# Optimization experiments

Hardware: AMD Instinct MI355X
Metric: run time of the kernel (lower is better)

Reference implementation:

```python
import jax, jax.numpy as jnp
import numpy as np

N = 50000   # nodes
E = 800000  # edges
D = 64      # attrs_dim
H = 128     # 2*attrs_dim (GIN MLP hidden)
L = 3       # gnn_layers_num
G = 128     # graphs in batch


def setup_inputs() -> dict:
    key = jax.random.key(0)
    ks = jax.random.split(key, 9)
    s = 0.1
    attrs = jax.random.normal(ks[0], (N, D), dtype=jnp.float32)
    edge_index = jax.random.randint(ks[1], (2, E), 0, N, dtype=jnp.int64)
    batch = jnp.sort(jax.random.randint(ks[2], (N,), 0, G, dtype=jnp.int64))
    W1 = jax.random.normal(ks[3], (L, D, H), dtype=jnp.float32) * s
    b1 = jnp.zeros((L, H), jnp.float32)
    W2 = jax.random.normal(ks[4], (L, H, H), dtype=jnp.float32) * s
    b2 = jnp.zeros((L, H), jnp.float32)
    W3 = jax.random.normal(ks[5], (L, H, D), dtype=jnp.float32) * s
    b3 = jnp.zeros((L, D), jnp.float32)
    return {"attrs": attrs, "W1": W1, "b1": b1, "W2": W2, "b2": b2,
            "W3": W3, "b3": b3, "edge_index": edge_index, "batch": batch}


def reference(attrs, W1, b1, W2, b2, W3, b3, edge_index, batch):
    src, dst = edge_index[0], edge_index[1]
    x = attrs
    for l in range(L):  # small fixed layer count
        # GINConv with eps=0: MLP(x + sum_{j->i} x_j)
        agg = jax.ops.segment_sum(x[src], dst, num_segments=N)
        h = x + agg
        # MLP with tanh after each linear (per MLP.forward)
        h = jnp.tanh(h @ W1[l] + b1[l])
        h = jnp.tanh(h @ W2[l] + b2[l])
        h = jnp.tanh(h @ W3[l] + b3[l])
        # outer activation in GNN.forward
        x = jnp.tanh(h)
    # scatter_mean over graph ids
    sums = jax.ops.segment_sum(x, batch, num_segments=G)          # [G, D]
    counts = jax.ops.segment_sum(jnp.ones((N,), x.dtype), batch, num_segments=G)
    return sums / jnp.maximum(counts, 1.0)[:, None]
```

## Files before the change

### kernel.cpp

```cpp
#include <hip/hip_runtime.h>
#include <math.h>

#define N_NODES 50000
#define N_EDGES 800000
#define DIM 64
#define HID 128
#define LAYERS 3
#define NGRAPH 128

#define SCAN_TILE 1024
#define SCAN_NB ((N_NODES + SCAN_TILE - 1) / SCAN_TILE)

#define POOL_ROWS 256
#define POOL_NB ((N_NODES + POOL_ROWS - 1) / POOL_ROWS)

typedef __attribute__((ext_vector_type(8))) short short8v;
typedef __attribute__((ext_vector_type(4))) float f32x4;

__device__ __forceinline__ float bf2f(unsigned short u) {
    return __uint_as_float(((unsigned)u) << 16);
}
__device__ __forceinline__ unsigned short f2bf(float x) {
    unsigned u = __float_as_uint(x);
    unsigned r = (u + 0x7fff + ((u >> 16) & 1)) >> 16;
    return (unsigned short)r;
}
__device__ __forceinline__ float fast_tanh(float x) {
    float xc = fminf(fmaxf(x, -9.0f), 9.0f);
    float y = __expf(2.0f * xc);
    return 1.0f - 2.0f * __builtin_amdgcn_rcpf(y + 1.0f);
}

__global__ void count_kernel(const int* __restrict__ dst,
                             int* __restrict__ counts,
                             unsigned short* __restrict__ rank) {
    int e = blockIdx.x * blockDim.x + threadIdx.x;
    if (e >= N_EDGES) return;
    rank[e] = (unsigned short)atomicAdd(&counts[dst[e]], 1);
}

__global__ void scan_partial_kernel(const int* __restrict__ counts,
                                    int* __restrict__ bsum) {
    __shared__ int red[256];
    const int b = blockIdx.x, tid = threadIdx.x;
    const int base = b * SCAN_TILE + tid * 4;
    int s = 0;
    if (base + 3 < N_NODES) {
        int4 v = *reinterpret_cast<const int4*>(counts + base);
        s = v.x + v.y + v.z + v.w;
    } else {
        for (int i = 0; i < 4; ++i)
            if (base + i < N_NODES) s += counts[base + i];
    }
    red[tid] = s;
    __syncthreads();
    for (int off = 128; off > 0; off >>= 1) {
        if (tid < off) red[tid] += red[tid + off];
        __syncthreads();
    }
    if (tid == 0) bsum[b] = red[0];
}

__global__ void scan_mid_kernel(const int* __restrict__ bsum,
                                int* __restrict__ bpre,
                                int* __restrict__ offsets) {
    int tid = threadIdx.x;
    int orig = (tid < SCAN_NB) ? bsum[tid] : 0;
    int v = orig;
    for (int off = 1; off < 64; off <<= 1) {
        int u = __shfl_up(v, off);
        if (tid >= off) v += u;
    }
    if (tid < SCAN_NB) bpre[tid] = v - orig;
    if (tid == 0) offsets[N_NODES] = N_EDGES;
}

__global__ void scan_final_kernel(const int* __restrict__ counts,
                                  const int* __restrict__ bpre,
                                  int* __restrict__ offsets) {
    __shared__ int pre[256];
    const int b = blockIdx.x, tid = threadIdx.x;
    const int base = b * SCAN_TILE + tid * 4;
    int c[4];
    int s = 0;
#pragma unroll
    for (int i = 0; i < 4; ++i) {
        c[i] = (base + i < N_NODES) ? counts[base + i] : 0;
        s += c[i];
    }
    pre[tid] = s;
    __syncthreads();
    for (int off = 1; off < 256; off <<= 1) {
        int v = (tid >= off) ? pre[tid - off] : 0;
        __syncthreads();
        pre[tid] += v;
        __syncthreads();
    }
    int run = bpre[b] + pre[tid] - s;
#pragma unroll
    for (int i = 0; i < 4; ++i) {
        if (base + i < N_NODES) {
            offsets[base + i] = run;
            run += c[i];
        }
    }
}

__global__ void place_kernel(const int* __restrict__ src,
                             const int* __restrict__ dst,
                             const unsigned short* __restrict__ rank,
                             const int* __restrict__ offsets,
                             unsigned short* __restrict__ csr_src) {
    int e = blockIdx.x * blockDim.x + threadIdx.x;
    if (e >= N_EDGES) return;
    csr_src[offsets[dst[e]] + (int)rank[e]] = (unsigned short)src[e];
}

template<int K, int C>
__global__ void repack_kernel(const float* __restrict__ W, unsigned short* __restrict__ P) {
    constexpr int KT = K / 32, CT = C / 16;
    int t = blockIdx.x * 256 + threadIdx.x;
    if (t >= LAYERS * KT * CT * 64) return;
    int lane = t & 63; int rest = t >> 6;
    int ct = rest % CT; rest /= CT;
    int kt = rest % KT; int l = rest / KT;
    int li = lane & 15, hi = lane >> 4;
    const float* Wl = W + (size_t)l * K * C;
    short8v o;
#pragma unroll
    for (int j = 0; j < 8; ++j)
        o[j] = (short)f2bf(Wl[(size_t)(kt * 32 + hi * 8 + j) * C + ct * 16 + li]);
    *reinterpret_cast<short8v*>(P + ((size_t)l * KT * CT * 64 + (size_t)(kt * CT + ct) * 64 + lane) * 8) = o;
}

template<bool F32IN>
__global__ __launch_bounds__(256) void gnn_layer_kernel(
        const float* __restrict__ xf, const unsigned short* __restrict__ xb,
        const int* __restrict__ offsets, const unsigned short* __restrict__ csr_src,
        const unsigned short* __restrict__ pw1, const float* __restrict__ bias1,
        const unsigned short* __restrict__ pw2, const float* __restrict__ bias2,
        const unsigned short* __restrict__ pw3, const float* __restrict__ bias3,
        unsigned short* __restrict__ outx) {
    __shared__ float aggA[16 * 68];
    __shared__ float aggB[16 * 68];
    __shared__ unsigned short tileA[16 * 128];
    __shared__ unsigned short tileB[16 * 128];
    __shared__ int soff[17];
    const int tid = threadIdx.x;
    const int wave = tid >> 6, lane = tid & 63;
    const int li = lane & 15, hi = lane >> 4;
    const int r0 = blockIdx.x * 16;
    char* tA = reinterpret_cast<char*>(tileA);
    char* tB = reinterpret_cast<char*>(tileB);

    if (tid < 17) soff[tid] = offsets[r0 + tid];
    __syncthreads();

    {
        const int g  = tid >> 3;
        const int nr = g >> 1;
        const int h  = g & 1;
        const int q  = tid & 7;
        const int n  = r0 + nr;
        float a[8];
        if (h == 0) {
            if (F32IN) {
                const float* xr = xf + (size_t)n * DIM + q * 8;
                float4 u = *reinterpret_cast<const float4*>(xr);
                float4 w = *reinterpret_cast<const float4*>(xr + 4);
                a[0]=u.x; a[1]=u.y; a[2]=u.z; a[3]=u.w;
                a[4]=w.x; a[5]=w.y; a[6]=w.z; a[7]=w.w;
            } else {
                short8v v = *reinterpret_cast<const short8v*>(xb + (size_t)n * DIM + q * 8);
#pragma unroll
                for (int j = 0; j < 8; ++j) a[j] = bf2f((unsigned short)v[j]);
            }
        } else {
#pragma unroll
            for (int j = 0; j < 8; ++j) a[j] = 0.f;
        }
        const int p0 = soff[nr], pe1 = soff[nr + 1];
        const int mid = p0 + ((pe1 - p0 + 1) >> 1);
        int p        = h ? mid : p0;
        const int pe = h ? pe1 : mid;
        for (; p + 4 <= pe; p += 4) {
            int s0 = csr_src[p + 0];
            int s1 = csr_src[p + 1];
            int s2 = csr_src[p + 2];
            int s3 = csr_src[p + 3];
            if (F32IN) {
                const float* x0 = xf + (size_t)s0 * DIM + q * 8;
                const float* x1 = xf + (size_t)s1 * DIM + q * 8;
                const float* x2 = xf + (size_t)s2 * DIM + q * 8;
                const float* x3 = xf + (size_t)s3 * DIM + q * 8;
                float4 u0 = *reinterpret_cast<const float4*>(x0);
                float4 w0 = *reinterpret_cast<const float4*>(x0 + 4);
                float4 u1 = *reinterpret_cast<const float4*>(x1);
                float4 w1 = *reinterpret_cast<const float4*>(x1 + 4);
                float4 u2 = *reinterpret_cast<const float4*>(x2);
                float4 w2 = *reinterpret_cast<const float4*>(x2 + 4);
                float4 u3 = *reinterpret_cast<const float4*>(x3);
                float4 w3 = *reinterpret_cast<const float4*>(x3 + 4);
                a[0] += u0.x + u1.x + u2.x + u3.x;
                a[1] += u0.y + u1.y + u2.y + u3.y;
                a[2] += u0.z + u1.z + u2.z + u3.z;
                a[3] += u0.w + u1.w + u2.w + u3.w;
                a[4] += w0.x + w1.x + w2.x + w3.x;
                a[5] += w0.y + w1.y + w2.y + w3.y;
                a[6] += w0.z + w1.z + w2.z + w3.z;
                a[7] += w0.w + w1.w + w2.w + w3.w;
            } else {
                short8v v0 = *reinterpret_cast<const short8v*>(xb + (size_t)s0 * DIM + q * 8);
                short8v v1 = *reinterpret_cast<const short8v*>(xb + (size_t)s1 * DIM + q * 8);
                short8v v2 = *reinterpret_cast<const short8v*>(xb + (size_t)s2 * DIM + q * 8);
                short8v v3 = *reinterpret_cast<const short8v*>(xb + (size_t)s3 * DIM + q * 8);
#pragma unroll
                for (int j = 0; j < 8; ++j)
                    a[j] += bf2f((unsigned short)v0[j]) + bf2f((unsigned short)v1[j])
                          + bf2f((unsigned short)v2[j]) + bf2f((unsigned short)v3[j]);
            }
        }
        for (; p < pe; ++p) {
            int s = csr_src[p];
            if (F32IN) {
                const float* xs = xf + (size_t)s * DIM + q * 8;
                float4 u = *reinterpret_cast<const float4*>(xs);
                float4 w = *reinterpret_cast<const float4*>(xs + 4);
                a[0] += u.x; a[1] += u.y; a[2] += u.z; a[3] += u.w;
                a[4] += w.x; a[5] += w.y; a[6] += w.z; a[7] += w.w;
            } else {
                short8v v = *reinterpret_cast<const short8v*>(xb + (size_t)s * DIM + q * 8);
#pragma unroll
                for (int j = 0; j < 8; ++j) a[j] += bf2f((unsigned short)v[j]);
            }
        }
        float* d = (h ? aggB : aggA) + nr * 68 + q * 8;
        *reinterpret_cast<f32x4*>(d)     = (f32x4){a[0], a[1], a[2], a[3]};
        *reinterpret_cast<f32x4*>(d + 4) = (f32x4){a[4], a[5], a[6], a[7]};
    }
    __syncthreads();

    short8v af[2];
#pragma unroll
    for (int kt = 0; kt < 2; ++kt) {
        const float* sA = &aggA[li * 68 + kt * 32 + hi * 8];
        const float* sB = &aggB[li * 68 + kt * 32 + hi * 8];
#pragma unroll
        for (int j = 0; j < 8; ++j) af[kt][j] = (short)f2bf(sA[j] + sB[j]);
    }

    f32x4 acc1[2];
#pragma unroll
    for (int c = 0; c < 2; ++c) acc1[c] = (f32x4){0.f, 0.f, 0.f, 0.f};
#pragma unroll
    for (int c = 0; c < 2; ++c) {
        const int ct = 2 * wave + c;
#pragma unroll
        for (int kt = 0; kt < 2; ++kt) {
            short8v bfr = *reinterpret_cast<const short8v*>(pw1 + ((size_t)(kt * 8 + ct) * 64 + lane) * 8);
            acc1[c] = __builtin_amdgcn_mfma_f32_16x16x32_bf16(af[kt], bfr, acc1[c], 0, 0, 0);
        }
    }
#pragma unroll
    for (int c = 0; c < 2; ++c) {
        const int ct = 2 * wave + c;
        float bv = bias1[ct * 16 + li];
#pragma unroll
        for (int j = 0; j < 4; ++j) {
            int row = hi * 4 + j;
            unsigned off = (unsigned)(row * 256 + (ct * 16 + li) * 2) ^ ((unsigned)(row & 7) << 4);
            *reinterpret_cast<unsigned short*>(tA + off) = f2bf(fast_tanh(acc1[c][j] + bv));
        }
    }
    __syncthreads();

    short8v af2[4];
#pragma unroll
    for (int kt = 0; kt < 4; ++kt) {
        unsigned off = (unsigned)(li * 256 + (kt * 32 + hi * 8) * 2) ^ ((unsigned)(li & 7) << 4);
        af2[kt] = *reinterpret_cast<const short8v*>(tA + off);
    }
    f32x4 acc2[2];
#pragma unroll
    for (int c = 0; c < 2; ++c) acc2[c] = (f32x4){0.f, 0.f, 0.f, 0.f};
#pragma unroll
    for (int c = 0; c < 2; ++c) {
        const int ct = 2 * wave + c;
#pragma unroll
        for (int kt = 0; kt < 4; ++kt) {
            short8v bfr = *reinterpret_cast<const short8v*>(pw2 + ((size_t)(kt * 8 + ct) * 64 + lane) * 8);
            acc2[c] = __builtin_amdgcn_mfma_f32_16x16x32_bf16(af2[kt], bfr, acc2[c], 0, 0, 0);
        }
    }
#pragma unroll
    for (int c = 0; c < 2; ++c) {
        const int ct = 2 * wave + c;
        float bv = bias2[ct * 16 + li];
#pragma unroll
        for (int j = 0; j < 4; ++j) {
            int row = hi * 4 + j;
            unsigned off = (unsigned)(row * 256 + (ct * 16 + li) * 2) ^ ((unsigned)(row & 7) << 4);
            *reinterpret_cast<unsigned short*>(tB + off) = f2bf(fast_tanh(acc2[c][j] + bv));
        }
    }
    __syncthreads();

    short8v af3[4];
#pragma unroll
    for (int kt = 0; kt < 4; ++kt) {
        unsigned off = (unsigned)(li * 256 + (kt * 32 + hi * 8) * 2) ^ ((unsigned)(li & 7) << 4);
        af3[kt] = *reinterpret_cast<const short8v*>(tB + off);
    }
    f32x4 acc3 = (f32x4){0.f, 0.f, 0.f, 0.f};
#pragma unroll
    for (int kt = 0; kt < 4; ++kt) {
        short8v bfr = *reinterpret_cast<const short8v*>(pw3 + ((size_t)(kt * 4 + wave) * 64 + lane) * 8);
        acc3 = __builtin_amdgcn_mfma_f32_16x16x32_bf16(af3[kt], bfr, acc3, 0, 0, 0);
    }
    {
        float bv = bias3[wave * 16 + li];
#pragma unroll
        for (int j = 0; j < 4; ++j) {
            int row = r0 + hi * 4 + j;
            float v = fast_tanh(fast_tanh(acc3[j] + bv));
            outx[(size_t)row * DIM + wave * 16 + li] = f2bf(v);
        }
    }
}

__global__ void pool_partial_kernel(const unsigned short* __restrict__ x,
                                    const int* __restrict__ batch,
                                    float* __restrict__ sums) {
    const int tid = threadIdx.x;
    const int d = tid & 63;
    const int rg = tid >> 6;
    int row = blockIdx.x * POOL_ROWS + rg;
    const int rowend = min(N_NODES, (blockIdx.x + 1) * POOL_ROWS);
    float acc = 0.f;
    int cur = -1;
    for (; row < rowend; row += 4) {
        int g = batch[row];
        if (g != cur) {
            if (cur >= 0) atomicAdd(&sums[cur * DIM + d], acc);
            acc = 0.f;
            cur = g;
        }
        acc += bf2f(x[(size_t)row * DIM + d]);
    }
    if (cur >= 0) atomicAdd(&sums[cur * DIM + d], acc);
}

__global__ void pool_final_kernel(const float* __restrict__ sums,
                                  const int* __restrict__ batch,
                                  float* __restrict__ out) {
    const int g = blockIdx.x;
    const int d = threadIdx.x;
    int lo = 0, hi = N_NODES;
    while (lo < hi) { int m = (lo + hi) >> 1; if (batch[m] < g) lo = m + 1; else hi = m; }
    int start = lo;
    hi = N_NODES;
    while (lo < hi) { int m = (lo + hi) >> 1; if (batch[m] < g + 1) lo = m + 1; else hi = m; }
    float cnt = (float)(lo - start);
    out[g * DIM + d] = sums[g * DIM + d] / fmaxf(cnt, 1.f);
}

extern "C" void kernel_launch(void* const* d_in, const int* in_sizes, int n_in,
                              void* d_out, int out_size, void* d_ws, size_t ws_size,
                              hipStream_t stream) {
    const float* attrs = (const float*)d_in[0];
    const float* W1    = (const float*)d_in[1];
    const float* b1    = (const float*)d_in[2];
    const float* W2    = (const float*)d_in[3];
    const float* b2    = (const float*)d_in[4];
    const float* W3    = (const float*)d_in[5];
    const float* b3    = (const float*)d_in[6];
    const int* edge_index = (const int*)d_in[7];
    const int* batch      = (const int*)d_in[8];
    float* out = (float*)d_out;

    unsigned short* buf0 = (unsigned short*)d_ws;
    unsigned short* buf1 = buf0 + (size_t)N_NODES * DIM;
    unsigned short* pW1  = buf1 + (size_t)N_NODES * DIM;
    unsigned short* pW2  = pW1 + 24576;
    unsigned short* pW3  = pW2 + 49152;
    float* psums  = (float*)(pW3 + 24576);
    int* offsets  = (int*)(psums + NGRAPH * DIM);
    unsigned short* csr16 = (unsigned short*)(offsets + N_NODES + 1);
    unsigned short* rank  = csr16 + N_EDGES;
    int* counts   = (int*)(rank + N_EDGES);
    int* bsum     = counts + N_NODES;
    int* bpre     = bsum + SCAN_NB;

    const int* src = edge_index;
    const int* dst = edge_index + N_EDGES;

    const int edge_blocks = (N_EDGES + 255) / 256;
    const int gnn_blocks  = N_NODES / 16;

    hipMemsetAsync(counts, 0, (size_t)N_NODES * sizeof(int), stream);
    count_kernel<<<edge_blocks, 256, 0, stream>>>(dst, counts, rank);
    scan_partial_kernel<<<SCAN_NB, 256, 0, stream>>>(counts, bsum);
    scan_mid_kernel<<<1, 64, 0, stream>>>(bsum, bpre, offsets);
    scan_final_kernel<<<SCAN_NB, 256, 0, stream>>>(counts, bpre, offsets);
    place_kernel<<<edge_blocks, 256, 0, stream>>>(src, dst, rank, offsets, csr16);

    repack_kernel<DIM, HID><<<(LAYERS * 2 * 8 * 64 + 255) / 256, 256, 0, stream>>>(W1, pW1);
    repack_kernel<HID, HID><<<(LAYERS * 4 * 8 * 64 + 255) / 256, 256, 0, stream>>>(W2, pW2);
    repack_kernel<HID, DIM><<<(LAYERS * 4 * 4 * 64 + 255) / 256, 256, 0, stream>>>(W3, pW3);

    for (int l = 0; l < LAYERS; ++l) {
        const unsigned short* w1 = pW1 + (size_t)l * 2 * 8 * 64 * 8;
        const unsigned short* w2 = pW2 + (size_t)l * 4 * 8 * 64 * 8;
        const unsigned short* w3 = pW3 + (size_t)l * 4 * 4 * 64 * 8;
        const float* bb1 = b1 + (size_t)l * HID;
        const float* bb2 = b2 + (size_t)l * HID;
        const float* bb3 = b3 + (size_t)l * DIM;
        if (l == 0)
            gnn_layer_kernel<true><<<gnn_blocks, 256, 0, stream>>>(
                attrs, nullptr, offsets, csr16, w1, bb1, w2, bb2, w3, bb3, buf0);
        else {
            const unsigned short* in = (l == 1) ? buf0 : buf1;
            unsigned short* outb     = (l == 1) ? buf1 : buf0;
            gnn_layer_kernel<false><<<gnn_blocks, 256, 0, stream>>>(
                nullptr, in, offsets, csr16, w1, bb1, w2, bb2, w3, bb3, outb);
        }
    }

    hipMemsetAsync(psums, 0, (size_t)NGRAPH * DIM * sizeof(float), stream);
    pool_partial_kernel<<<POOL_NB, 256, 0, stream>>>(buf0, batch, psums);
    pool_final_kernel<<<NGRAPH, DIM, 0, stream>>>(psums, batch, out);
}
```

Before: 186.7 us.

## Fuse mean-pool into last GNN layer, merge repack launches, two edges per count thread

The last GNN layer now accumulates its output straight into per-graph sums with atomics instead of writing a bf16 buffer and running a separate pool kernel. The three weight-repack launches are merged into one kernel, and the count kernel handles two edges per thread. The aim is to remove launches and an extra pass over node features. The cost is many more global float atomics from the last layer, one per 4-row group per column, and pooling now sums fp32 values rather than bf16-rounded ones.

Result: no change. 183.4 us (-1.8%).

```diff
diff --git a/kernel.cpp b/kernel.cpp
--- a/kernel.cpp
+++ b/kernel.cpp
@@ -11,9 +11,6 @@
 #define SCAN_TILE 1024
 #define SCAN_NB ((N_NODES + SCAN_TILE - 1) / SCAN_TILE)
 
-#define POOL_ROWS 256
-#define POOL_NB ((N_NODES + POOL_ROWS - 1) / POOL_ROWS)
-
 typedef __attribute__((ext_vector_type(8))) short short8v;
 typedef __attribute__((ext_vector_type(4))) float f32x4;
 
@@ -34,9 +31,16 @@
 __global__ void count_kernel(const int* __restrict__ dst,
                              int* __restrict__ counts,
                              unsigned short* __restrict__ rank) {
-    int e = blockIdx.x * blockDim.x + threadIdx.x;
-    if (e >= N_EDGES) return;
-    rank[e] = (unsigned short)atomicAdd(&counts[dst[e]], 1);
+    int e = (blockIdx.x * blockDim.x + threadIdx.x) * 2;
+    if (e + 1 < N_EDGES) {
+        int d0 = dst[e], d1 = dst[e + 1];
+        int r0 = atomicAdd(&counts[d0], 1);
+        int r1 = atomicAdd(&counts[d1], 1);
+        rank[e]     = (unsigned short)r0;
+        rank[e + 1] = (unsigned short)r1;
+    } else if (e < N_EDGES) {
+        rank[e] = (unsigned short)atomicAdd(&counts[dst[e]], 1);
+    }
 }
 
 __global__ void scan_partial_kernel(const int* __restrict__ counts,
@@ -117,10 +121,9 @@
 }
 
 template<int K, int C>
-__global__ void repack_kernel(const float* __restrict__ W, unsigned short* __restrict__ P) {
+__device__ __forceinline__ void repack_one(const float* __restrict__ W,
+                                           unsigned short* __restrict__ P, int t) {
     constexpr int KT = K / 32, CT = C / 16;
-    int t = blockIdx.x * 256 + threadIdx.x;
-    if (t >= LAYERS * KT * CT * 64) return;
     int lane = t & 63; int rest = t >> 6;
     int ct = rest % CT; rest /= CT;
     int kt = rest % KT; int l = rest / KT;
@@ -133,14 +136,25 @@
     *reinterpret_cast<short8v*>(P + ((size_t)l * KT * CT * 64 + (size_t)(kt * CT + ct) * 64 + lane) * 8) = o;
 }
 
-template<bool F32IN>
+__global__ void repack_all_kernel(const float* __restrict__ W1, const float* __restrict__ W2,
+                                  const float* __restrict__ W3,
+                                  unsigned short* __restrict__ P1, unsigned short* __restrict__ P2,
+                                  unsigned short* __restrict__ P3) {
+    int t = blockIdx.x * 256 + threadIdx.x;
+    if (t < 3072)       repack_one<DIM, HID>(W1, P1, t);
+    else if (t < 9216)  repack_one<HID, HID>(W2, P2, t - 3072);
+    else                repack_one<HID, DIM>(W3, P3, t - 9216);
+}
+
+template<bool F32IN, bool LAST>
 __global__ __launch_bounds__(256) void gnn_layer_kernel(
         const float* __restrict__ xf, const unsigned short* __restrict__ xb,
         const int* __restrict__ offsets, const unsigned short* __restrict__ csr_src,
         const unsigned short* __restrict__ pw1, const float* __restrict__ bias1,
         const unsigned short* __restrict__ pw2, const float* __restrict__ bias2,
         const unsigned short* __restrict__ pw3, const float* __restrict__ bias3,
-        unsigned short* __restrict__ outx) {
+        unsigned short* __restrict__ outx,
+        const int* __restrict__ batch, float* __restrict__ psums) {
     __shared__ float aggA[16 * 68];
     __shared__ float aggB[16 * 68];
     __shared__ unsigned short tileA[16 * 128];
@@ -318,36 +332,34 @@
         acc3 = __builtin_amdgcn_mfma_f32_16x16x32_bf16(af3[kt], bfr, acc3, 0, 0, 0);
     }
     {
-        float bv = bias3[wave * 16 + li];
-#pragma unroll
-        for (int j = 0; j < 4; ++j) {
-            int row = r0 + hi * 4 + j;
-            float v = fast_tanh(fast_tanh(acc3[j] + bv));
-            outx[(size_t)row * DIM + wave * 16 + li] = f2bf(v);
-        }
-    }
-}
-
-__global__ void pool_partial_kernel(const unsigned short* __restrict__ x,
-                                    const int* __restrict__ batch,
-                                    float* __restrict__ sums) {
-    const int tid = threadIdx.x;
-    const int d = tid & 63;
-    const int rg = tid >> 6;
-    int row = blockIdx.x * POOL_ROWS + rg;
-    const int rowend = min(N_NODES, (blockIdx.x + 1) * POOL_ROWS);
-    float acc = 0.f;
-    int cur = -1;
-    for (; row < rowend; row += 4) {
-        int g = batch[row];
-        if (g != cur) {
-            if (cur >= 0) atomicAdd(&sums[cur * DIM + d], acc);
-            acc = 0.f;
-            cur = g;
-        }
-        acc += bf2f(x[(size_t)row * DIM + d]);
-    }
-    if (cur >= 0) atomicAdd(&sums[cur * DIM + d], acc);
+        const int c = wave * 16 + li;
+        float bv = bias3[c];
+        if (LAST) {
+            const int row0 = r0 + hi * 4;
+            float v[4];
+#pragma unroll
+            for (int j = 0; j < 4; ++j) v[j] = fast_tanh(fast_tanh(acc3[j] + bv));
+            int g = batch[row0];
+            float acc = v[0];
+#pragma unroll
+            for (int j = 1; j < 4; ++j) {
+                int gj = batch[row0 + j];
+                if (gj == g) acc += v[j];
+                else {
+                    atomicAdd(&psums[g * DIM + c], acc);
+                    g = gj; acc = v[j];
+                }
+            }
+            atomicAdd(&psums[g * DIM + c], acc);
+        } else {
+#pragma unroll
+            for (int j = 0; j < 4; ++j) {
+                int row = r0 + hi * 4 + j;
+                float vv = fast_tanh(fast_tanh(acc3[j] + bv));
+                outx[(size_t)row * DIM + c] = f2bf(vv);
+            }
+        }
+    }
 }
 
 __global__ void pool_final_kernel(const float* __restrict__ sums,
@@ -394,19 +406,19 @@
     const int* src = edge_index;
     const int* dst = edge_index + N_EDGES;
 
-    const int edge_blocks = (N_EDGES + 255) / 256;
-    const int gnn_blocks  = N_NODES / 16;
+    const int edge_blocks  = (N_EDGES + 255) / 256;
+    const int count_blocks = (N_EDGES / 2 + 255) / 256;
+    const int gnn_blocks   = N_NODES / 16;
 
     hipMemsetAsync(counts, 0, (size_t)N_NODES * sizeof(int), stream);
-    count_kernel<<<edge_blocks, 256, 0, stream>>>(dst, counts, rank);
+    hipMemsetAsync(psums, 0, (size_t)NGRAPH * DIM * sizeof(float), stream);
+    count_kernel<<<count_blocks, 256, 0, stream>>>(dst, counts, rank);
     scan_partial_kernel<<<SCAN_NB, 256, 0, stream>>>(counts, bsum);
     scan_mid_kernel<<<1, 64, 0, stream>>>(bsum, bpre, offsets);
     scan_final_kernel<<<SCAN_NB, 256, 0, stream>>>(counts, bpre, offsets);
     place_kernel<<<edge_blocks, 256, 0, stream>>>(src, dst, rank, offsets, csr16);
 
-    repack_kernel<DIM, HID><<<(LAYERS * 2 * 8 * 64 + 255) / 256, 256, 0, stream>>>(W1, pW1);
-    repack_kernel<HID, HID><<<(LAYERS * 4 * 8 * 64 + 255) / 256, 256, 0, stream>>>(W2, pW2);
-    repack_kernel<HID, DIM><<<(LAYERS * 4 * 4 * 64 + 255) / 256, 256, 0, stream>>>(W3, pW3);
+    repack_all_kernel<<<48, 256, 0, stream>>>(W1, W2, W3, pW1, pW2, pW3);
 
     for (int l = 0; l < LAYERS; ++l) {
         const unsigned short* w1 = pW1 + (size_t)l * 2 * 8 * 64 * 8;
@@ -416,17 +428,18 @@
         const float* bb2 = b2 + (size_t)l * HID;
         const float* bb3 = b3 + (size_t)l * DIM;
         if (l == 0)
-            gnn_layer_kernel<true><<<gnn_blocks, 256, 0, stream>>>(
-                attrs, nullptr, offsets, csr16, w1, bb1, w2, bb2, w3, bb3, buf0);
-        else {
-            const unsigned short* in = (l == 1) ? buf0 : buf1;
-            unsigned short* outb     = (l == 1) ? buf1 : buf0;
-            gnn_layer_kernel<false><<<gnn_blocks, 256, 0, stream>>>(
-                nullptr, in, offsets, csr16, w1, bb1, w2, bb2, w3, bb3, outb);
-        }
-    }
-
-    hipMemsetAsync(psums, 0, (size_t)NGRAPH * DIM * sizeof(float), stream);
-    pool_partial_kernel<<<POOL_NB, 256, 0, stream>>>(buf0, batch, psums);
+            gnn_layer_kernel<true, false><<<gnn_blocks, 256, 0, stream>>>(
+                attrs, nullptr, offsets, csr16, w1, bb1, w2, bb2, w3, bb3,
+                buf0, nullptr, nullptr);
+        else if (l == 1)
+            gnn_layer_kernel<false, false><<<gnn_blocks, 256, 0, stream>>>(
+                nullptr, buf0, offsets, csr16, w1, bb1, w2, bb2, w3, bb3,
+                buf1, nullptr, nullptr);
+        else
+            gnn_layer_kernel<false, true><<<gnn_blocks, 256, 0, stream>>>(
+                nullptr, buf1, offsets, csr16, w1, bb1, w2, bb2, w3, bb3,
+                nullptr, batch, psums);
+    }
+
     pool_final_kernel<<<NGRAPH, DIM, 0, stream>>>(psums, batch, out);
 }
```
